# Performance work log

Measured on AMD Instinct MI355X. Metric: run time of the kernel, lower is better.

## Reference

```python
import jax, jax.numpy as jnp
import numpy as np

N_NODES = 100000
N_EDGES = 1600000
D = 128
NUM_LAYERS = 2
EPS = 1e-5


def setup_inputs() -> dict:
    key = jax.random.key(0)
    ks = jax.random.split(key, 8)
    s = 1.0 / np.sqrt(D)
    x = jax.random.normal(ks[0], (N_NODES, D), dtype=jnp.float32)
    edge_index = jax.random.randint(ks[1], (2, N_EDGES), 0, N_NODES, dtype=jnp.int64)
    W1 = jax.random.uniform(ks[2], (D, D), jnp.float32, -s, s)
    b1 = jnp.zeros((D,), jnp.float32)
    W2 = jax.random.uniform(ks[3], (D, D), jnp.float32, -s, s)
    b2 = jnp.zeros((D,), jnp.float32)
    inner = (NUM_LAYERS + 1) * D
    bn_gamma = jnp.ones((inner,), jnp.float32)
    bn_beta = jnp.zeros((inner,), jnp.float32)
    so = 1.0 / np.sqrt(inner)
    Wo = jax.random.uniform(ks[4], (inner, D), jnp.float32, -so, so)
    bo = jax.random.uniform(ks[5], (D,), jnp.float32, -so, so)
    return dict(x=x, edge_index=edge_index, W1=W1, b1=b1, W2=W2, b2=b2,
                bn_gamma=bn_gamma, bn_beta=bn_beta, Wo=Wo, bo=bo)


def gcn_conv(x, src, dst, W, b, n_nodes):
    """PyG GCNConv: symmetric norm with added self-loops, linear then aggregate."""
    h = x @ W  # [N, D]
    deg = jax.ops.segment_sum(jnp.ones_like(src, dtype=h.dtype), dst,
                              num_segments=n_nodes) + 1.0  # +1 self-loop
    dinv = jax.lax.rsqrt(deg)  # deg >= 1 so finite
    norm = dinv[src] * dinv[dst]  # [E]
    msg = h[src] * norm[:, None]  # gather: memory-bound
    agg = jax.ops.segment_sum(msg, dst, num_segments=n_nodes)
    agg = agg + h * (dinv * dinv)[:, None]  # self-loop message
    return agg + b


def reference(x, edge_index, W1, b1, W2, b2, bn_gamma, bn_beta, Wo, bo):
    src, dst = edge_index[0], edge_index[1]
    n = x.shape[0]
    x_cat = [x]
    h = jax.nn.relu(gcn_conv(x, src, dst, W1, b1, n))
    x_cat.append(h)
    h = jax.nn.relu(gcn_conv(h, src, dst, W2, b2, n))
    x_cat.append(h)
    xc = jnp.concatenate(x_cat, axis=-1)  # [N, 3D]
    # BatchNorm1d (training forward: batch statistics, biased variance)
    mu = jnp.mean(xc, axis=0)
    var = jnp.mean(jnp.square(xc - mu), axis=0)
    xn = (xc - mu) * jax.lax.rsqrt(var + EPS) * bn_gamma + bn_beta
    return xn @ Wo + bo  # [N, D]
```

## Files before the change

### kernel.cpp

```cpp
#include <hip/hip_runtime.h>
#include <hip/hip_bf16.h>

#define DD 128
#define NBLK 256
#define MAXBUK 1024
#define CAP2 12288

typedef __attribute__((ext_vector_type(8))) short bf16x8;
typedef __attribute__((ext_vector_type(4))) float f32x4;
typedef unsigned int uint32;

__device__ __forceinline__ unsigned short f2b(float f) {
  __hip_bfloat16 h = __float2bfloat16(f);
  unsigned short u;
  __builtin_memcpy(&u, &h, 2);
  return u;
}
__device__ __forceinline__ float b2f_lo(uint32 v) { return __uint_as_float(v << 16); }
__device__ __forceinline__ float b2f_hi(uint32 v) { return __uint_as_float(v & 0xffff0000u); }

__device__ __forceinline__ void acc8(float* acc, uint4 h, float w) {
  acc[0] = fmaf(w, b2f_lo(h.x), acc[0]);
  acc[1] = fmaf(w, b2f_hi(h.x), acc[1]);
  acc[2] = fmaf(w, b2f_lo(h.y), acc[2]);
  acc[3] = fmaf(w, b2f_hi(h.y), acc[3]);
  acc[4] = fmaf(w, b2f_lo(h.z), acc[4]);
  acc[5] = fmaf(w, b2f_hi(h.z), acc[5]);
  acc[6] = fmaf(w, b2f_lo(h.w), acc[6]);
  acc[7] = fmaf(w, b2f_hi(h.w), acc[7]);
}

__global__ void k_detect(const int* __restrict__ e, int pairs, int* __restrict__ flag) {
  __shared__ int nz;
  if (threadIdx.x == 0) nz = 0;
  __syncthreads();
  int samples = pairs < 4096 ? pairs : 4096;
  for (int i = threadIdx.x; i < samples; i += blockDim.x)
    if (e[2 * i + 1] != 0) atomicAdd(&nz, 1);
  __syncthreads();
  if (threadIdx.x == 0) *flag = (nz == 0) ? 1 : 0;
}

__global__ __launch_bounds__(256) void k_hist(const void* __restrict__ eptr, int E,
                                              const int* __restrict__ flag,
                                              int* __restrict__ degi, int* __restrict__ histT,
                                              int nbuk, int dohist) {
  __shared__ int hist[MAXBUK];
  int t = threadIdx.x, blk = blockIdx.x;
  if (dohist)
    for (int b = t; b < nbuk; b += 256) hist[b] = 0;
  __syncthreads();
  int chunk = (E + NBLK - 1) / NBLK;
  int i0 = blk * chunk, i1 = min(E, i0 + chunk);
  bool f = (*flag) != 0;
  for (int i = i0 + t; i < i1; i += 256) {
    int dst = f ? (int)((const long long*)eptr)[E + i] : ((const int*)eptr)[E + i];
    atomicAdd(&degi[dst], 1);
    if (dohist) atomicAdd(&hist[dst >> 8], 1);
  }
  __syncthreads();
  if (dohist)
    for (int b = t; b < nbuk; b += 256) histT[b * NBLK + blk] = hist[b];
}

__global__ void k_scan1(const int* __restrict__ cnt, int* __restrict__ rp,
                        int* __restrict__ bsum, int n, float* __restrict__ dinv) {
  __shared__ int ws[4];
  int t = threadIdx.x, lane = t & 63, wv = t >> 6;
  int i = blockIdx.x * 256 + t;
  int v = (i < n) ? cnt[i] : 0;
  if (i < n) dinv[i] = rsqrtf((float)v + 1.0f);
  int incl = v;
#pragma unroll
  for (int o = 1; o < 64; o <<= 1) {
    int u = __shfl_up(incl, o);
    if (lane >= o) incl += u;
  }
  if (lane == 63) ws[wv] = incl;
  __syncthreads();
  int off = 0;
  for (int k = 0; k < wv; ++k) off += ws[k];
  if (i < n) rp[i] = incl - v + off;
  if (t == 255) bsum[blockIdx.x] = off + incl;
}

__global__ void k_scan2(const int* __restrict__ cnt, int* __restrict__ rp, int n) {
  __shared__ int wsum[16];
  __shared__ int ctot;
  int t = threadIdx.x, lane = t & 63, wid = t >> 6;
  int base = 0;
  for (int start = 0; start < n; start += 1024) {
    int i = start + t;
    int v = (i < n) ? cnt[i] : 0;
    int incl = v;
#pragma unroll
    for (int o = 1; o < 64; o <<= 1) {
      int u = __shfl_up(incl, o);
      if (lane >= o) incl += u;
    }
    if (lane == 63) wsum[wid] = incl;
    __syncthreads();
    if (t < 16) {
      int s = wsum[t];
      int e = s;
#pragma unroll
      for (int o = 1; o < 16; o <<= 1) {
        int u = __shfl_up(e, o, 16);
        if (t >= o) e += u;
      }
      wsum[t] = e - s;
      if (t == 15) ctot = e;
    }
    __syncthreads();
    if (i < n) rp[i] = base + wsum[wid] + incl - v;
    base += ctot;
    __syncthreads();
  }
  if (t == 0) rp[n] = base;
}

__global__ void k_scan3(int* __restrict__ rp, const int* __restrict__ bsumex, int n, int nb) {
  int i = blockIdx.x * 256 + threadIdx.x;
  if (i < n) rp[i] += bsumex[blockIdx.x];
  if (i == 0) rp[n] = bsumex[nb];
}

__global__ void k_bscan(const int* __restrict__ histT, const int* __restrict__ rp,
                        int* __restrict__ offs, int nbuk) {
  int t = threadIdx.x, lane = t & 63, wid = t >> 6;
  int b = blockIdx.x * 4 + wid;
  if (b >= nbuk) return;
  int base = rp[b << 8];
  int idx = b * NBLK + lane * 4;
  int v0 = histT[idx], v1 = histT[idx + 1], v2 = histT[idx + 2], v3 = histT[idx + 3];
  int lsum = v0 + v1 + v2 + v3;
  int incl = lsum;
#pragma unroll
  for (int o = 1; o < 64; o <<= 1) {
    int u = __shfl_up(incl, o);
    if (lane >= o) incl += u;
  }
  int excl = base + incl - lsum;
  offs[idx] = excl;
  offs[idx + 1] = excl + v0;
  offs[idx + 2] = excl + v0 + v1;
  offs[idx + 3] = excl + v0 + v1 + v2;
}

__global__ __launch_bounds__(256) void k_place(const void* __restrict__ eptr, int E,
                                               const int* __restrict__ flag,
                                               const int* __restrict__ offs,
                                               int* __restrict__ ebuk, int nbuk) {
  __shared__ int cur[MAXBUK];
  int t = threadIdx.x, blk = blockIdx.x;
  for (int b = t; b < nbuk; b += 256) cur[b] = offs[b * NBLK + blk];
  __syncthreads();
  int chunk = (E + NBLK - 1) / NBLK;
  int i0 = blk * chunk, i1 = min(E, i0 + chunk);
  bool f = (*flag) != 0;
  for (int i = i0 + t; i < i1; i += 256) {
    int src, dst;
    if (f) {
      src = (int)((const long long*)eptr)[i];
      dst = (int)((const long long*)eptr)[E + i];
    } else {
      src = ((const int*)eptr)[i];
      dst = ((const int*)eptr)[E + i];
    }
    int pos = atomicAdd(&cur[dst >> 8], 1);
    ebuk[pos] = (src << 8) | (dst & 255);
  }
}

__global__ __launch_bounds__(256) void k_bsort(const int* __restrict__ ebuk,
                                               const int* __restrict__ rp,
                                               int* __restrict__ csrc, int n, int nbuk) {
  __shared__ int curs[256];
  __shared__ int outb[CAP2];
  int b = blockIdx.x, t = threadIdx.x;
  int v0 = b << 8;
  int v1 = min(v0 + 256, n);
  int base = rp[v0];
  int cnt = rp[v1] - base;
  int nn = v1 - v0;
  if (t < nn) curs[t] = rp[v0 + t] - base;
  __syncthreads();
  if (cnt <= CAP2) {
    for (int i = t; i < cnt; i += 256) {
      int e = ebuk[base + i];
      int slot = atomicAdd(&curs[e & 255], 1);
      outb[slot] = e >> 8;
    }
    __syncthreads();
    for (int i = t; i < cnt; i += 256) csrc[base + i] = outb[i];
  } else {
    for (int i = t; i < cnt; i += 256) {
      int e = ebuk[base + i];
      int slot = atomicAdd(&curs[e & 255], 1);
      csrc[base + slot] = e >> 8;
    }
  }
}

__global__ void k_scatter_fb(const void* __restrict__ eptr, int E, const int* __restrict__ flag,
                             const int* __restrict__ rp, int* __restrict__ cur,
                             int* __restrict__ csrc) {
  int i = blockIdx.x * 256 + threadIdx.x;
  if (i >= E) return;
  bool f = (*flag) != 0;
  int src, dst;
  if (f) {
    src = (int)((const long long*)eptr)[i];
    dst = (int)((const long long*)eptr)[E + i];
  } else {
    src = ((const int*)eptr)[i];
    dst = ((const int*)eptr)[E + i];
  }
  int pos = rp[dst] + atomicAdd(&cur[dst], 1);
  csrc[pos] = src;
}

__global__ __launch_bounds__(256) void k_cvt_x(const float4* __restrict__ x,
                                               ushort4* __restrict__ xb, int n4,
                                               float* __restrict__ part) {
  int t = threadIdx.x;
  float s[4] = {0, 0, 0, 0}, q[4] = {0, 0, 0, 0};
  for (int i = blockIdx.x * 256 + t; i < n4; i += gridDim.x * 256) {
    float4 a = x[i];
    ushort4 o;
    o.x = f2b(a.x); o.y = f2b(a.y); o.z = f2b(a.z); o.w = f2b(a.w);
    xb[i] = o;
    s[0] += a.x; s[1] += a.y; s[2] += a.z; s[3] += a.w;
    q[0] = fmaf(a.x, a.x, q[0]); q[1] = fmaf(a.y, a.y, q[1]);
    q[2] = fmaf(a.z, a.z, q[2]); q[3] = fmaf(a.w, a.w, q[3]);
  }
  __shared__ float sh[256][8];
#pragma unroll
  for (int j = 0; j < 4; ++j) { sh[t][j] = s[j]; sh[t][4 + j] = q[j]; }
  __syncthreads();
  if (t < 32) {
#pragma unroll
    for (int g = 1; g < 8; ++g)
#pragma unroll
      for (int j = 0; j < 4; ++j) {
        s[j] += sh[g * 32 + t][j];
        q[j] += sh[g * 32 + t][4 + j];
      }
    float* pp = part + (size_t)(blockIdx.x & 63) * 768;
#pragma unroll
    for (int j = 0; j < 4; ++j) {
      atomicAdd(&pp[(t * 4 + j) * 2], s[j]);
      atomicAdd(&pp[(t * 4 + j) * 2 + 1], q[j]);
    }
  }
}

__global__ void k_prep_w(const float* __restrict__ W1, const float* __restrict__ W2,
                         unsigned short* __restrict__ wimg) {
  int i = blockIdx.x * 256 + threadIdx.x;
  if (i >= 32768) return;
  int wsel = i >> 14;
  int j = i & 16383;
  int k = j >> 7, col = j & 127;
  float v = (wsel ? W2 : W1)[j];
  int chunk = (k >> 3) ^ (col & 7);
  wimg[wsel * 16384 + col * 128 + chunk * 8 + (k & 7)] = f2b(v);
}

__global__ __launch_bounds__(256) void k_gemm(const unsigned short* __restrict__ Ab,
                                              const unsigned short* __restrict__ Wimg,
                                              const float* __restrict__ dinv,
                                              unsigned short* __restrict__ H, int n) {
  __shared__ __align__(16) unsigned short Wl[16384];
  int t = threadIdx.x, lane = t & 63, w = t >> 6;
#pragma unroll
  for (int i = t; i < 2048; i += 256) ((int4*)Wl)[i] = ((const int4*)Wimg)[i];
  __syncthreads();
  int rowBase = blockIdx.x * 128 + w * 32;
  int r16 = lane & 15, half = lane >> 4;
  f32x4 acc[2][8];
#pragma unroll
  for (int m = 0; m < 2; ++m)
#pragma unroll
    for (int nn = 0; nn < 8; ++nn) acc[m][nn] = (f32x4){0.f, 0.f, 0.f, 0.f};
#pragma unroll
  for (int ks = 0; ks < 4; ++ks) {
    bf16x8 a[2];
#pragma unroll
    for (int m = 0; m < 2; ++m) {
      int r = rowBase + m * 16 + r16;
      if (r >= n) r = n - 1;
      a[m] = *(const bf16x8*)(Ab + (size_t)r * DD + ks * 32 + half * 8);
    }
#pragma unroll
    for (int nn = 0; nn < 8; ++nn) {
      int col = nn * 16 + r16;
      int chunk = (ks * 4 + half) ^ (col & 7);
      bf16x8 b = *(const bf16x8*)(Wl + col * 128 + chunk * 8);
      acc[0][nn] = __builtin_amdgcn_mfma_f32_16x16x32_bf16(a[0], b, acc[0][nn], 0, 0, 0);
      acc[1][nn] = __builtin_amdgcn_mfma_f32_16x16x32_bf16(a[1], b, acc[1][nn], 0, 0, 0);
    }
  }
#pragma unroll
  for (int m = 0; m < 2; ++m) {
    int rb = rowBase + m * 16 + half * 4;
    float dv[4];
#pragma unroll
    for (int i = 0; i < 4; ++i) dv[i] = (rb + i < n) ? dinv[rb + i] : 0.f;
#pragma unroll
    for (int nn = 0; nn < 8; ++nn) {
      int col = nn * 16 + r16;
#pragma unroll
      for (int i = 0; i < 4; ++i) {
        int r = rb + i;
        if (r < n) H[(size_t)r * DD + col] = f2b(acc[m][nn][i] * dv[i]);
      }
    }
  }
}

__global__ __launch_bounds__(256) void k_agg(const unsigned short* __restrict__ hs,
                                             const float* __restrict__ dinv,
                                             const float* __restrict__ b,
                                             const int* __restrict__ rp,
                                             const int* __restrict__ csrc,
                                             unsigned short* __restrict__ y, int n,
                                             float* __restrict__ part, int cb) {
  __shared__ float sh_s[8][128];
  __shared__ float sh_q[8][128];
  int wid = threadIdx.x >> 6, lane = threadIdx.x & 63;
  int eidx = lane >> 4;
  int seg = lane & 15;
  int vA = blockIdx.x * 8 + wid;
  int vB = vA + 4;
  bool okA = vA < n, okB = vB < n;
  int a0 = 0, b0 = 0, a1 = 0, b1 = 0;
  if (okA) { a0 = rp[vA]; b0 = rp[vA + 1]; }
  if (okB) { a1 = rp[vB]; b1 = rp[vB + 1]; }
  const uint4* H4 = (const uint4*)hs;
  uint4 selfA = okA ? H4[(size_t)vA * 16 + seg] : make_uint4(0, 0, 0, 0);
  uint4 selfB = okB ? H4[(size_t)vB * 16 + seg] : make_uint4(0, 0, 0, 0);
  float accA[8], accB[8];
#pragma unroll
  for (int j = 0; j < 8; ++j) { accA[j] = 0.f; accB[j] = 0.f; }
  int ebA = a0, ebB = a1;
  while (ebA < b0 || ebB < b1) {
    int ecA = b0 - ebA; ecA = ecA < 0 ? 0 : (ecA > 64 ? 64 : ecA);
    int ecB = b1 - ebB; ecB = ecB < 0 ? 0 : (ecB > 64 ? 64 : ecB);
    int ulA = (ebA + lane < b0) ? csrc[ebA + lane] : 0;
    int ulB = (ebB + lane < b1) ? csrc[ebB + lane] : 0;
    int iters = ecA > ecB ? ecA : ecB;
    for (int cc = 0; cc < iters; cc += 16) {
      int uA0 = __shfl(ulA, cc + eidx), uA1 = __shfl(ulA, cc + 4 + eidx);
      int uA2 = __shfl(ulA, cc + 8 + eidx), uA3 = __shfl(ulA, cc + 12 + eidx);
      int uB0 = __shfl(ulB, cc + eidx), uB1 = __shfl(ulB, cc + 4 + eidx);
      int uB2 = __shfl(ulB, cc + 8 + eidx), uB3 = __shfl(ulB, cc + 12 + eidx);
      float wA0 = (cc + eidx < ecA) ? 1.f : 0.f;
      float wA1 = (cc + 4 + eidx < ecA) ? 1.f : 0.f;
      float wA2 = (cc + 8 + eidx < ecA) ? 1.f : 0.f;
      float wA3 = (cc + 12 + eidx < ecA) ? 1.f : 0.f;
      float wB0 = (cc + eidx < ecB) ? 1.f : 0.f;
      float wB1 = (cc + 4 + eidx < ecB) ? 1.f : 0.f;
      float wB2 = (cc + 8 + eidx < ecB) ? 1.f : 0.f;
      float wB3 = (cc + 12 + eidx < ecB) ? 1.f : 0.f;
      uint4 hA0 = H4[(size_t)uA0 * 16 + seg];
      uint4 hA1 = H4[(size_t)uA1 * 16 + seg];
      uint4 hA2 = H4[(size_t)uA2 * 16 + seg];
      uint4 hA3 = H4[(size_t)uA3 * 16 + seg];
      uint4 hB0 = H4[(size_t)uB0 * 16 + seg];
      uint4 hB1 = H4[(size_t)uB1 * 16 + seg];
      uint4 hB2 = H4[(size_t)uB2 * 16 + seg];
      uint4 hB3 = H4[(size_t)uB3 * 16 + seg];
      acc8(accA, hA0, wA0); acc8(accA, hA1, wA1);
      acc8(accA, hA2, wA2); acc8(accA, hA3, wA3);
      acc8(accB, hB0, wB0); acc8(accB, hB1, wB1);
      acc8(accB, hB2, wB2); acc8(accB, hB3, wB3);
    }
    ebA += 64;
    ebB += 64;
  }
#pragma unroll
  for (int j = 0; j < 8; ++j) {
    accA[j] += __shfl_xor(accA[j], 16);
    accA[j] += __shfl_xor(accA[j], 32);
    accB[j] += __shfl_xor(accB[j], 16);
    accB[j] += __shfl_xor(accB[j], 32);
  }
  float4 bb0 = ((const float4*)b)[seg * 2];
  float4 bb1 = ((const float4*)b)[seg * 2 + 1];
  float bv[8] = {bb0.x, bb0.y, bb0.z, bb0.w, bb1.x, bb1.y, bb1.z, bb1.w};
  float oA[8], oB[8];
  if (okA) {
    float sf[8] = {b2f_lo(selfA.x), b2f_hi(selfA.x), b2f_lo(selfA.y), b2f_hi(selfA.y),
                   b2f_lo(selfA.z), b2f_hi(selfA.z), b2f_lo(selfA.w), b2f_hi(selfA.w)};
    float dv = dinv[vA];
#pragma unroll
    for (int j = 0; j < 8; ++j) oA[j] = fmaxf(fmaf(dv, accA[j] + sf[j], bv[j]), 0.f);
    if (eidx == 0) {
      uint4 ov;
      ov.x = (uint32)f2b(oA[0]) | ((uint32)f2b(oA[1]) << 16);
      ov.y = (uint32)f2b(oA[2]) | ((uint32)f2b(oA[3]) << 16);
      ov.z = (uint32)f2b(oA[4]) | ((uint32)f2b(oA[5]) << 16);
      ov.w = (uint32)f2b(oA[6]) | ((uint32)f2b(oA[7]) << 16);
      ((uint4*)y)[(size_t)vA * 16 + seg] = ov;
    }
  } else {
#pragma unroll
    for (int j = 0; j < 8; ++j) oA[j] = 0.f;
  }
  if (okB) {
    float sf[8] = {b2f_lo(selfB.x), b2f_hi(selfB.x), b2f_lo(selfB.y), b2f_hi(selfB.y),
                   b2f_lo(selfB.z), b2f_hi(selfB.z), b2f_lo(selfB.w), b2f_hi(selfB.w)};
    float dv = dinv[vB];
#pragma unroll
    for (int j = 0; j < 8; ++j) oB[j] = fmaxf(fmaf(dv, accB[j] + sf[j], bv[j]), 0.f);
    if (eidx == 0) {
      uint4 ov;
      ov.x = (uint32)f2b(oB[0]) | ((uint32)f2b(oB[1]) << 16);
      ov.y = (uint32)f2b(oB[2]) | ((uint32)f2b(oB[3]) << 16);
      ov.z = (uint32)f2b(oB[4]) | ((uint32)f2b(oB[5]) << 16);
      ov.w = (uint32)f2b(oB[6]) | ((uint32)f2b(oB[7]) << 16);
      ((uint4*)y)[(size_t)vB * 16 + seg] = ov;
    }
  } else {
#pragma unroll
    for (int j = 0; j < 8; ++j) oB[j] = 0.f;
  }
  if (eidx == 0) {
#pragma unroll
    for (int j = 0; j < 8; ++j) {
      sh_s[wid][seg * 8 + j] = oA[j];
      sh_q[wid][seg * 8 + j] = oA[j] * oA[j];
      sh_s[wid + 4][seg * 8 + j] = oB[j];
      sh_q[wid + 4][seg * 8 + j] = oB[j] * oB[j];
    }
  }
  __syncthreads();
  if (threadIdx.x < 128) {
    int c = threadIdx.x;
    float s = 0.f, q = 0.f;
#pragma unroll
    for (int k2 = 0; k2 < 8; ++k2) {
      s += sh_s[k2][c];
      q += sh_q[k2][c];
    }
    float* pp = part + (size_t)(blockIdx.x & 63) * 768;
    atomicAdd(&pp[(cb + c) * 2], s);
    atomicAdd(&pp[(cb + c) * 2 + 1], q);
  }
}

__global__ void k_fold_a(const float* __restrict__ part, const float* __restrict__ gamma,
                         const float* __restrict__ beta, const float* __restrict__ Wo,
                         const float* __restrict__ bo, float* __restrict__ aS,
                         float* __restrict__ boP, int n) {
  __shared__ float cSh[384];
  int t = threadIdx.x;
  float s = 0.f, q = 0.f;
  for (int r = 0; r < 64; ++r) {
    s += part[r * 768 + t * 2];
    q += part[r * 768 + t * 2 + 1];
  }
  float inv_n = 1.0f / (float)n;
  float mu = s * inv_n;
  float var = q * inv_n - mu * mu;
  float a = gamma[t] * rsqrtf(var + 1e-5f);
  aS[t] = a;
  cSh[t] = beta[t] - mu * a;
  __syncthreads();
  if (t < DD) {
    float sb = bo[t];
    for (int k = 0; k < 384; ++k) sb = fmaf(cSh[k], Wo[k * DD + t], sb);
    boP[t] = sb;
  }
}

__global__ void k_foldw(const float* __restrict__ aS, const float* __restrict__ Wo,
                        unsigned short* __restrict__ wopimg) {
  int i = blockIdx.x * 256 + threadIdx.x;
  if (i >= 49152) return;
  int krow = i >> 7, col = i & 127;
  float v = aS[krow] * Wo[i];
  int p = krow >> 7, kk = krow & 127;
  int chunk = (kk >> 3) ^ (col & 7);
  wopimg[p * 16384 + col * 128 + chunk * 8 + (kk & 7)] = f2b(v);
}

__global__ __launch_bounds__(256) void k_gemm_out(const unsigned short* __restrict__ xb,
                                                  const unsigned short* __restrict__ y1,
                                                  const unsigned short* __restrict__ y2,
                                                  const unsigned short* __restrict__ Wimg3,
                                                  const float* __restrict__ boP,
                                                  float* __restrict__ out, int n) {
  __shared__ __align__(16) unsigned short Wl[16384];
  int t = threadIdx.x, lane = t & 63, w = t >> 6;
  int rowBase = blockIdx.x * 128 + w * 32;
  int r16 = lane & 15, half = lane >> 4;
  f32x4 acc[2][8];
#pragma unroll
  for (int m = 0; m < 2; ++m)
#pragma unroll
    for (int nn = 0; nn < 8; ++nn) acc[m][nn] = (f32x4){0.f, 0.f, 0.f, 0.f};
  for (int p = 0; p < 3; ++p) {
    const unsigned short* Ab = (p == 0) ? xb : (p == 1) ? y1 : y2;
    __syncthreads();
#pragma unroll
    for (int i = t; i < 2048; i += 256) ((int4*)Wl)[i] = ((const int4*)(Wimg3 + p * 16384))[i];
    __syncthreads();
#pragma unroll
    for (int ks = 0; ks < 4; ++ks) {
      bf16x8 a[2];
#pragma unroll
      for (int m = 0; m < 2; ++m) {
        int r = rowBase + m * 16 + r16;
        if (r >= n) r = n - 1;
        a[m] = *(const bf16x8*)(Ab + (size_t)r * DD + ks * 32 + half * 8);
      }
#pragma unroll
      for (int nn = 0; nn < 8; ++nn) {
        int col = nn * 16 + r16;
        int chunk = (ks * 4 + half) ^ (col & 7);
        bf16x8 b = *(const bf16x8*)(Wl + col * 128 + chunk * 8);
        acc[0][nn] = __builtin_amdgcn_mfma_f32_16x16x32_bf16(a[0], b, acc[0][nn], 0, 0, 0);
        acc[1][nn] = __builtin_amdgcn_mfma_f32_16x16x32_bf16(a[1], b, acc[1][nn], 0, 0, 0);
      }
    }
  }
#pragma unroll
  for (int m = 0; m < 2; ++m) {
    int rb = rowBase + m * 16 + half * 4;
#pragma unroll
    for (int nn = 0; nn < 8; ++nn) {
      int col = nn * 16 + r16;
      float bb = boP[col];
#pragma unroll
      for (int i = 0; i < 4; ++i) {
        int r = rb + i;
        if (r < n) out[(size_t)r * DD + col] = acc[m][nn][i] + bb;
      }
    }
  }
}

extern "C" void kernel_launch(void* const* d_in, const int* in_sizes, int n_in,
                              void* d_out, int out_size, void* d_ws, size_t ws_size,
                              hipStream_t stream) {
  const float* x = (const float*)d_in[0];
  const void* ept = d_in[1];
  const float* W1 = (const float*)d_in[2];
  const float* b1 = (const float*)d_in[3];
  const float* W2 = (const float*)d_in[4];
  const float* b2 = (const float*)d_in[5];
  const float* gamma = (const float*)d_in[6];
  const float* beta = (const float*)d_in[7];
  const float* Wo = (const float*)d_in[8];
  const float* bo = (const float*)d_in[9];
  float* out = (float*)d_out;
  int N = in_sizes[0] / DD;
  int E = in_sizes[1] / 2;
  int nbuk = (N + 255) >> 8;

  char* w = (char*)d_ws;
  size_t off = 0;
  auto alloc = [&](size_t bytes) {
    void* p = w + off;
    off = (off + bytes + 255) & ~(size_t)255;
    return p;
  };
  float* dinv = (float*)alloc((size_t)N * 4);
  int* degi = (int*)alloc((size_t)N * 4);
  int* rp = (int*)alloc((size_t)(N + 1) * 4);
  int* csrc = (int*)alloc((size_t)E * 4);
  int* ebuk = (int*)alloc((size_t)E * 4);
  int* histT = (int*)alloc((size_t)MAXBUK * NBLK * 4);
  int* offs = (int*)alloc((size_t)MAXBUK * NBLK * 4);
  unsigned short* xb = (unsigned short*)alloc((size_t)N * DD * 2);
  unsigned short* h = (unsigned short*)alloc((size_t)N * DD * 2);
  unsigned short* y1 = (unsigned short*)alloc((size_t)N * DD * 2);
  unsigned short* y2 = (unsigned short*)alloc((size_t)N * DD * 2);
  unsigned short* wimg = (unsigned short*)alloc(32768 * 2);
  unsigned short* wopimg = (unsigned short*)alloc(49152 * 2);
  float* part = (float*)alloc((size_t)64 * 768 * 4);
  float* aS = (float*)alloc(384 * 4);
  float* boP = (float*)alloc(DD * 4);
  int* flag = (int*)alloc(4);
  int nbs = (N + 255) / 256;
  int* bsum = (int*)alloc((size_t)(nbs + 1) * 4);

  int dohist = (nbuk <= MAXBUK) ? 1 : 0;

  hipMemsetAsync(degi, 0, (size_t)N * 4, stream);
  hipMemsetAsync(part, 0, (size_t)64 * 768 * 4, stream);

  int eb = (E + 255) / 256;
  k_detect<<<1, 256, 0, stream>>>((const int*)ept, E, flag);
  k_hist<<<NBLK, 256, 0, stream>>>(ept, E, flag, degi, histT, nbuk, dohist);
  k_scan1<<<nbs, 256, 0, stream>>>(degi, rp, bsum, N, dinv);
  k_scan2<<<1, 1024, 0, stream>>>(bsum, bsum, nbs);
  k_scan3<<<nbs, 256, 0, stream>>>(rp, bsum, N, nbs);
  if (dohist) {
    k_bscan<<<(nbuk + 3) / 4, 256, 0, stream>>>(histT, rp, offs, nbuk);
    k_place<<<NBLK, 256, 0, stream>>>(ept, E, flag, offs, ebuk, nbuk);
    k_bsort<<<nbuk, 256, 0, stream>>>(ebuk, rp, csrc, N, nbuk);
  } else {
    hipMemsetAsync(degi, 0, (size_t)N * 4, stream);
    k_scatter_fb<<<eb, 256, 0, stream>>>(ept, E, flag, rp, degi, csrc);
  }

  int n4 = N * DD / 4;
  k_cvt_x<<<1024, 256, 0, stream>>>((const float4*)x, (ushort4*)xb, n4, part);
  k_prep_w<<<128, 256, 0, stream>>>(W1, W2, wimg);

  int gb = (N + 127) / 128;
  int ab = (N + 7) / 8;
  k_gemm<<<gb, 256, 0, stream>>>(xb, wimg, dinv, h, N);
  k_agg<<<ab, 256, 0, stream>>>(h, dinv, b1, rp, csrc, y1, N, part, 128);
  k_gemm<<<gb, 256, 0, stream>>>(y1, wimg + 16384, dinv, h, N);
  k_agg<<<ab, 256, 0, stream>>>(h, dinv, b2, rp, csrc, y2, N, part, 256);

  k_fold_a<<<1, 384, 0, stream>>>(part, gamma, beta, Wo, bo, aS, boP, N);
  k_foldw<<<192, 256, 0, stream>>>(aS, Wo, wopimg);
  k_gemm_out<<<gb, 256, 0, stream>>>(xb, y1, y2, wopimg, boP, out, N);
}
```

Before: 385.8 us.

## Restructure CSR build to compute degrees per bucket and fuse preprocessing kernels

Removes the global per-node degree atomics and the three-kernel node-level scan. Bucket totals are now scanned in a single kernel, and each bucket-sort block counts its own per-node degrees, so rowptr and dinv are derived locally. The i64 detection is inlined with a wave ballot, and the x/weight conversion kernels are merged into one launch, cutting several launches and one memset. The no-histogram fallback path is dropped, so more than MAXBUK buckets (N > 262144) is no longer handled, and detection now samples only 64 edges.

```diff
diff --git a/kernel.cpp b/kernel.cpp
--- a/kernel.cpp
+++ b/kernel.cpp
@@ -30,134 +30,88 @@
   acc[7] = fmaf(w, b2f_hi(h.w), acc[7]);
 }
 
-__global__ void k_detect(const int* __restrict__ e, int pairs, int* __restrict__ flag) {
-  __shared__ int nz;
-  if (threadIdx.x == 0) nz = 0;
-  __syncthreads();
-  int samples = pairs < 4096 ? pairs : 4096;
-  for (int i = threadIdx.x; i < samples; i += blockDim.x)
-    if (e[2 * i + 1] != 0) atomicAdd(&nz, 1);
-  __syncthreads();
-  if (threadIdx.x == 0) *flag = (nz == 0) ? 1 : 0;
+__device__ __forceinline__ bool detect_i64(const int* e, int E) {
+  int lane = threadIdx.x & 63;
+  int samples = E < 64 ? E : 64;
+  int v = (lane < samples) ? e[2 * lane + 1] : 0;
+  return __ballot(v != 0) == 0ULL;
 }
 
 __global__ __launch_bounds__(256) void k_hist(const void* __restrict__ eptr, int E,
-                                              const int* __restrict__ flag,
-                                              int* __restrict__ degi, int* __restrict__ histT,
-                                              int nbuk, int dohist) {
+                                              int* __restrict__ histT, int nbuk) {
   __shared__ int hist[MAXBUK];
   int t = threadIdx.x, blk = blockIdx.x;
-  if (dohist)
-    for (int b = t; b < nbuk; b += 256) hist[b] = 0;
+  bool f = detect_i64((const int*)eptr, E);
+  for (int b = t; b < nbuk; b += 256) hist[b] = 0;
   __syncthreads();
   int chunk = (E + NBLK - 1) / NBLK;
   int i0 = blk * chunk, i1 = min(E, i0 + chunk);
-  bool f = (*flag) != 0;
   for (int i = i0 + t; i < i1; i += 256) {
     int dst = f ? (int)((const long long*)eptr)[E + i] : ((const int*)eptr)[E + i];
-    atomicAdd(&degi[dst], 1);
-    if (dohist) atomicAdd(&hist[dst >> 8], 1);
-  }
-  __syncthreads();
-  if (dohist)
-    for (int b = t; b < nbuk; b += 256) histT[b * NBLK + blk] = hist[b];
-}
-
-__global__ void k_scan1(const int* __restrict__ cnt, int* __restrict__ rp,
-                        int* __restrict__ bsum, int n, float* __restrict__ dinv) {
-  __shared__ int ws[4];
+    atomicAdd(&hist[dst >> 8], 1);
+  }
+  __syncthreads();
+  for (int b = t; b < nbuk; b += 256) histT[b * NBLK + blk] = hist[b];
+}
+
+__global__ __launch_bounds__(1024) void k_bktscan(const int* __restrict__ histT,
+                                                  int* __restrict__ offs,
+                                                  int* __restrict__ bucketBase,
+                                                  int nbuk, int E) {
+  __shared__ int tot[MAXBUK];
   int t = threadIdx.x, lane = t & 63, wv = t >> 6;
-  int i = blockIdx.x * 256 + t;
-  int v = (i < n) ? cnt[i] : 0;
-  if (i < n) dinv[i] = rsqrtf((float)v + 1.0f);
-  int incl = v;
-#pragma unroll
-  for (int o = 1; o < 64; o <<= 1) {
-    int u = __shfl_up(incl, o);
-    if (lane >= o) incl += u;
-  }
-  if (lane == 63) ws[wv] = incl;
-  __syncthreads();
-  int off = 0;
-  for (int k = 0; k < wv; ++k) off += ws[k];
-  if (i < n) rp[i] = incl - v + off;
-  if (t == 255) bsum[blockIdx.x] = off + incl;
-}
-
-__global__ void k_scan2(const int* __restrict__ cnt, int* __restrict__ rp, int n) {
-  __shared__ int wsum[16];
-  __shared__ int ctot;
-  int t = threadIdx.x, lane = t & 63, wid = t >> 6;
-  int base = 0;
-  for (int start = 0; start < n; start += 1024) {
-    int i = start + t;
-    int v = (i < n) ? cnt[i] : 0;
-    int incl = v;
+  for (int b = t; b < MAXBUK; b += 1024) tot[b] = 0;
+  __syncthreads();
+  for (int b = wv; b < nbuk; b += 16) {
+    const int4 vv = *(const int4*)(histT + b * NBLK + lane * 4);
+    int lsum = vv.x + vv.y + vv.z + vv.w;
+    int s = lsum;
 #pragma unroll
     for (int o = 1; o < 64; o <<= 1) {
-      int u = __shfl_up(incl, o);
-      if (lane >= o) incl += u;
-    }
-    if (lane == 63) wsum[wid] = incl;
+      int u = __shfl_up(s, o);
+      if (lane >= o) s += u;
+    }
+    if (lane == 63) tot[b] = s;
+  }
+  __syncthreads();
+  for (int o = 1; o < MAXBUK; o <<= 1) {
+    int u = (t >= o) ? tot[t - o] : 0;
     __syncthreads();
-    if (t < 16) {
-      int s = wsum[t];
-      int e = s;
-#pragma unroll
-      for (int o = 1; o < 16; o <<= 1) {
-        int u = __shfl_up(e, o, 16);
-        if (t >= o) e += u;
-      }
-      wsum[t] = e - s;
-      if (t == 15) ctot = e;
-    }
+    tot[t] += u;
     __syncthreads();
-    if (i < n) rp[i] = base + wsum[wid] + incl - v;
-    base += ctot;
-    __syncthreads();
-  }
-  if (t == 0) rp[n] = base;
-}
-
-__global__ void k_scan3(int* __restrict__ rp, const int* __restrict__ bsumex, int n, int nb) {
-  int i = blockIdx.x * 256 + threadIdx.x;
-  if (i < n) rp[i] += bsumex[blockIdx.x];
-  if (i == 0) rp[n] = bsumex[nb];
-}
-
-__global__ void k_bscan(const int* __restrict__ histT, const int* __restrict__ rp,
-                        int* __restrict__ offs, int nbuk) {
-  int t = threadIdx.x, lane = t & 63, wid = t >> 6;
-  int b = blockIdx.x * 4 + wid;
-  if (b >= nbuk) return;
-  int base = rp[b << 8];
-  int idx = b * NBLK + lane * 4;
-  int v0 = histT[idx], v1 = histT[idx + 1], v2 = histT[idx + 2], v3 = histT[idx + 3];
-  int lsum = v0 + v1 + v2 + v3;
-  int incl = lsum;
-#pragma unroll
-  for (int o = 1; o < 64; o <<= 1) {
-    int u = __shfl_up(incl, o);
-    if (lane >= o) incl += u;
-  }
-  int excl = base + incl - lsum;
-  offs[idx] = excl;
-  offs[idx + 1] = excl + v0;
-  offs[idx + 2] = excl + v0 + v1;
-  offs[idx + 3] = excl + v0 + v1 + v2;
+  }
+  for (int b = wv; b < nbuk; b += 16) {
+    int idx = b * NBLK + lane * 4;
+    const int4 vv = *(const int4*)(histT + idx);
+    int lsum = vv.x + vv.y + vv.z + vv.w;
+    int s = lsum;
+#pragma unroll
+    for (int o = 1; o < 64; o <<= 1) {
+      int u = __shfl_up(s, o);
+      if (lane >= o) s += u;
+    }
+    int tb = __shfl(s, 63);
+    int bbase = tot[b] - tb;
+    int excl = bbase + s - lsum;
+    offs[idx] = excl;
+    offs[idx + 1] = excl + vv.x;
+    offs[idx + 2] = excl + vv.x + vv.y;
+    offs[idx + 3] = excl + vv.x + vv.y + vv.z;
+    if (lane == 0) bucketBase[b] = bbase;
+  }
+  if (t == 0) bucketBase[nbuk] = E;
 }
 
 __global__ __launch_bounds__(256) void k_place(const void* __restrict__ eptr, int E,
-                                               const int* __restrict__ flag,
                                                const int* __restrict__ offs,
                                                int* __restrict__ ebuk, int nbuk) {
   __shared__ int cur[MAXBUK];
   int t = threadIdx.x, blk = blockIdx.x;
+  bool f = detect_i64((const int*)eptr, E);
   for (int b = t; b < nbuk; b += 256) cur[b] = offs[b * NBLK + blk];
   __syncthreads();
   int chunk = (E + NBLK - 1) / NBLK;
   int i0 = blk * chunk, i1 = min(E, i0 + chunk);
-  bool f = (*flag) != 0;
   for (int i = i0 + t; i < i1; i += 256) {
     int src, dst;
     if (f) {
@@ -172,60 +126,83 @@
   }
 }
 
-__global__ __launch_bounds__(256) void k_bsort(const int* __restrict__ ebuk,
-                                               const int* __restrict__ rp,
-                                               int* __restrict__ csrc, int n, int nbuk) {
-  __shared__ int curs[256];
+__global__ __launch_bounds__(256) void k_bsort2(const int* __restrict__ ebuk,
+                                                const int* __restrict__ bucketBase,
+                                                int* __restrict__ rp, float* __restrict__ dinv,
+                                                int* __restrict__ csrc, int n) {
+  __shared__ int cnt[256];
+  __shared__ int wss[4];
   __shared__ int outb[CAP2];
-  int b = blockIdx.x, t = threadIdx.x;
+  int b = blockIdx.x, t = threadIdx.x, lane = t & 63, wv = t >> 6;
   int v0 = b << 8;
   int v1 = min(v0 + 256, n);
-  int base = rp[v0];
-  int cnt = rp[v1] - base;
   int nn = v1 - v0;
-  if (t < nn) curs[t] = rp[v0 + t] - base;
-  __syncthreads();
-  if (cnt <= CAP2) {
-    for (int i = t; i < cnt; i += 256) {
+  int base = bucketBase[b];
+  int total = bucketBase[b + 1] - base;
+  cnt[t] = 0;
+  __syncthreads();
+  for (int i = t; i < total; i += 256) atomicAdd(&cnt[ebuk[base + i] & 255], 1);
+  __syncthreads();
+  int v = cnt[t];
+  int incl = v;
+#pragma unroll
+  for (int o = 1; o < 64; o <<= 1) {
+    int u = __shfl_up(incl, o);
+    if (lane >= o) incl += u;
+  }
+  if (lane == 63) wss[wv] = incl;
+  __syncthreads();
+  int woff = 0;
+  for (int k = 0; k < wv; ++k) woff += wss[k];
+  int excl = woff + incl - v;
+  if (t < nn) {
+    rp[v0 + t] = base + excl;
+    dinv[v0 + t] = rsqrtf((float)v + 1.0f);
+  }
+  if (t == 255) rp[v1] = base + excl + v;
+  __syncthreads();
+  cnt[t] = excl;
+  __syncthreads();
+  if (total <= CAP2) {
+    for (int i = t; i < total; i += 256) {
       int e = ebuk[base + i];
-      int slot = atomicAdd(&curs[e & 255], 1);
+      int slot = atomicAdd(&cnt[e & 255], 1);
       outb[slot] = e >> 8;
     }
     __syncthreads();
-    for (int i = t; i < cnt; i += 256) csrc[base + i] = outb[i];
+    for (int i = t; i < total; i += 256) csrc[base + i] = outb[i];
   } else {
-    for (int i = t; i < cnt; i += 256) {
+    for (int i = t; i < total; i += 256) {
       int e = ebuk[base + i];
-      int slot = atomicAdd(&curs[e & 255], 1);
+      int slot = atomicAdd(&cnt[e & 255], 1);
       csrc[base + slot] = e >> 8;
     }
   }
 }
 
-__global__ void k_scatter_fb(const void* __restrict__ eptr, int E, const int* __restrict__ flag,
-                             const int* __restrict__ rp, int* __restrict__ cur,
-                             int* __restrict__ csrc) {
-  int i = blockIdx.x * 256 + threadIdx.x;
-  if (i >= E) return;
-  bool f = (*flag) != 0;
-  int src, dst;
-  if (f) {
-    src = (int)((const long long*)eptr)[i];
-    dst = (int)((const long long*)eptr)[E + i];
-  } else {
-    src = ((const int*)eptr)[i];
-    dst = ((const int*)eptr)[E + i];
-  }
-  int pos = rp[dst] + atomicAdd(&cur[dst], 1);
-  csrc[pos] = src;
-}
-
-__global__ __launch_bounds__(256) void k_cvt_x(const float4* __restrict__ x,
-                                               ushort4* __restrict__ xb, int n4,
-                                               float* __restrict__ part) {
+__global__ __launch_bounds__(256) void k_cvtw(const float4* __restrict__ x,
+                                              ushort4* __restrict__ xb, int n4,
+                                              float* __restrict__ part,
+                                              const float* __restrict__ W1,
+                                              const float* __restrict__ W2,
+                                              unsigned short* __restrict__ wimg) {
+  __shared__ float sh[256][8];
   int t = threadIdx.x;
+  int bid = blockIdx.x;
+  if (bid >= 1024) {
+    int i = (bid - 1024) * 256 + t;
+    if (i < 32768) {
+      int wsel = i >> 14;
+      int j = i & 16383;
+      int k = j >> 7, col = j & 127;
+      float v = (wsel ? W2 : W1)[j];
+      int chunk = (k >> 3) ^ (col & 7);
+      wimg[wsel * 16384 + col * 128 + chunk * 8 + (k & 7)] = f2b(v);
+    }
+    return;
+  }
   float s[4] = {0, 0, 0, 0}, q[4] = {0, 0, 0, 0};
-  for (int i = blockIdx.x * 256 + t; i < n4; i += gridDim.x * 256) {
+  for (int i = bid * 256 + t; i < n4; i += 1024 * 256) {
     float4 a = x[i];
     ushort4 o;
     o.x = f2b(a.x); o.y = f2b(a.y); o.z = f2b(a.z); o.w = f2b(a.w);
@@ -234,7 +211,6 @@
     q[0] = fmaf(a.x, a.x, q[0]); q[1] = fmaf(a.y, a.y, q[1]);
     q[2] = fmaf(a.z, a.z, q[2]); q[3] = fmaf(a.w, a.w, q[3]);
   }
-  __shared__ float sh[256][8];
 #pragma unroll
   for (int j = 0; j < 4; ++j) { sh[t][j] = s[j]; sh[t][4 + j] = q[j]; }
   __syncthreads();
@@ -246,25 +222,13 @@
         s[j] += sh[g * 32 + t][j];
         q[j] += sh[g * 32 + t][4 + j];
       }
-    float* pp = part + (size_t)(blockIdx.x & 63) * 768;
+    float* pp = part + (size_t)(bid & 63) * 768;
 #pragma unroll
     for (int j = 0; j < 4; ++j) {
       atomicAdd(&pp[(t * 4 + j) * 2], s[j]);
       atomicAdd(&pp[(t * 4 + j) * 2 + 1], q[j]);
     }
   }
-}
-
-__global__ void k_prep_w(const float* __restrict__ W1, const float* __restrict__ W2,
-                         unsigned short* __restrict__ wimg) {
-  int i = blockIdx.x * 256 + threadIdx.x;
-  if (i >= 32768) return;
-  int wsel = i >> 14;
-  int j = i & 16383;
-  int k = j >> 7, col = j & 127;
-  float v = (wsel ? W2 : W1)[j];
-  int chunk = (k >> 3) ^ (col & 7);
-  wimg[wsel * 16384 + col * 128 + chunk * 8 + (k & 7)] = f2b(v);
 }
 
 __global__ __launch_bounds__(256) void k_gemm(const unsigned short* __restrict__ Ab,
@@ -568,12 +532,12 @@
     return p;
   };
   float* dinv = (float*)alloc((size_t)N * 4);
-  int* degi = (int*)alloc((size_t)N * 4);
   int* rp = (int*)alloc((size_t)(N + 1) * 4);
   int* csrc = (int*)alloc((size_t)E * 4);
   int* ebuk = (int*)alloc((size_t)E * 4);
   int* histT = (int*)alloc((size_t)MAXBUK * NBLK * 4);
   int* offs = (int*)alloc((size_t)MAXBUK * NBLK * 4);
+  int* bucketBase = (int*)alloc((size_t)(MAXBUK + 1) * 4);
   unsigned short* xb = (unsigned short*)alloc((size_t)N * DD * 2);
   unsigned short* h = (unsigned short*)alloc((size_t)N * DD * 2);
   unsigned short* y1 = (unsigned short*)alloc((size_t)N * DD * 2);
@@ -583,33 +547,16 @@
   float* part = (float*)alloc((size_t)64 * 768 * 4);
   float* aS = (float*)alloc(384 * 4);
   float* boP = (float*)alloc(DD * 4);
-  int* flag = (int*)alloc(4);
-  int nbs = (N + 255) / 256;
-  int* bsum = (int*)alloc((size_t)(nbs + 1) * 4);
-
-  int dohist = (nbuk <= MAXBUK) ? 1 : 0;
-
-  hipMemsetAsync(degi, 0, (size_t)N * 4, stream);
+
   hipMemsetAsync(part, 0, (size_t)64 * 768 * 4, stream);
 
-  int eb = (E + 255) / 256;
-  k_detect<<<1, 256, 0, stream>>>((const int*)ept, E, flag);
-  k_hist<<<NBLK, 256, 0, stream>>>(ept, E, flag, degi, histT, nbuk, dohist);
-  k_scan1<<<nbs, 256, 0, stream>>>(degi, rp, bsum, N, dinv);
-  k_scan2<<<1, 1024, 0, stream>>>(bsum, bsum, nbs);
-  k_scan3<<<nbs, 256, 0, stream>>>(rp, bsum, N, nbs);
-  if (dohist) {
-    k_bscan<<<(nbuk + 3) / 4, 256, 0, stream>>>(histT, rp, offs, nbuk);
-    k_place<<<NBLK, 256, 0, stream>>>(ept, E, flag, offs, ebuk, nbuk);
-    k_bsort<<<nbuk, 256, 0, stream>>>(ebuk, rp, csrc, N, nbuk);
-  } else {
-    hipMemsetAsync(degi, 0, (size_t)N * 4, stream);
-    k_scatter_fb<<<eb, 256, 0, stream>>>(ept, E, flag, rp, degi, csrc);
-  }
+  k_hist<<<NBLK, 256, 0, stream>>>(ept, E, histT, nbuk);
+  k_bktscan<<<1, 1024, 0, stream>>>(histT, offs, bucketBase, nbuk, E);
+  k_place<<<NBLK, 256, 0, stream>>>(ept, E, offs, ebuk, nbuk);
+  k_bsort2<<<nbuk, 256, 0, stream>>>(ebuk, bucketBase, rp, dinv, csrc, N);
 
   int n4 = N * DD / 4;
-  k_cvt_x<<<1024, 256, 0, stream>>>((const float4*)x, (ushort4*)xb, n4, part);
-  k_prep_w<<<128, 256, 0, stream>>>(W1, W2, wimg);
+  k_cvtw<<<1024 + 128, 256, 0, stream>>>((const float4*)x, (ushort4*)xb, n4, part, W1, W2, wimg);
 
   int gb = (N + 127) / 128;
   int ab = (N + 7) / 8;
```

New measurement: 340.1 us. -11.8%, faster.
